# Kernel tuning notes

Hardware: AMD Instinct MI355X
Metric: run time of the kernel (lower is better)

## Reference

```python
import jax, jax.numpy as jnp
import numpy as np

N = 100_000      # nodes
E = 3_200_000    # edges (avg degree 32)
D_IN = 64        # input node feature dim == lin3 out_dim (max over x_dict)
D_EDGE = 16      # edge feature dim
H = 16           # hidden_dim (also skip1 out = 16)


def setup_inputs() -> dict:
    key = jax.random.key(0)
    ks = jax.random.split(key, 12)
    x = jax.random.normal(ks[0], (N, D_IN), dtype=jnp.float32)
    edge_index = jax.random.randint(ks[1], (2, E), 0, N, dtype=jnp.int32)
    edge_attr = jax.random.normal(ks[2], (E, D_EDGE), dtype=jnp.float32)
    s = 0.05
    # conv1: message MLP over concat(x_src, edge_attr): (D_IN+D_EDGE) -> H
    W_msg1 = jax.random.normal(ks[3], (D_IN + D_EDGE, H), dtype=jnp.float32) * s
    b_msg1 = jnp.zeros((H,), dtype=jnp.float32)
    W_skip1 = jax.random.normal(ks[4], (D_IN, H), dtype=jnp.float32) * s
    b_skip1 = jnp.zeros((H,), dtype=jnp.float32)
    # conv2: concat(h_src, edge_attr): (H+D_EDGE) -> H
    W_msg2 = jax.random.normal(ks[5], (H + D_EDGE, H), dtype=jnp.float32) * s
    b_msg2 = jnp.zeros((H,), dtype=jnp.float32)
    W_skip2 = jax.random.normal(ks[6], (H, H), dtype=jnp.float32) * s
    b_skip2 = jnp.zeros((H,), dtype=jnp.float32)
    W_lin3 = jax.random.normal(ks[7], (H, D_IN), dtype=jnp.float32) * s
    b_lin3 = jnp.zeros((D_IN,), dtype=jnp.float32)
    return {
        "x": x, "edge_index": edge_index, "edge_attr": edge_attr,
        "W_msg1": W_msg1, "b_msg1": b_msg1, "W_skip1": W_skip1, "b_skip1": b_skip1,
        "W_msg2": W_msg2, "b_msg2": b_msg2, "W_skip2": W_skip2, "b_skip2": b_skip2,
        "W_lin3": W_lin3, "b_lin3": b_lin3,
    }


def _edge_conv(h, src, dst, edge_attr, W, b, num_nodes):
    # gather -> per-edge linear -> scatter-add at destination
    m = jnp.concatenate([h[src], edge_attr], axis=-1) @ W + b  # [E, H]
    return jax.ops.segment_sum(m, dst, num_segments=num_nodes)  # [N, H]


def reference(x, edge_index, edge_attr,
              W_msg1, b_msg1, W_skip1, b_skip1,
              W_msg2, b_msg2, W_skip2, b_skip2,
              W_lin3, b_lin3):
    src, dst = edge_index[0], edge_index[1]
    n = x.shape[0]
    h = _edge_conv(x, src, dst, edge_attr, W_msg1, b_msg1, n) + (x @ W_skip1 + b_skip1)
    h = jax.nn.relu(h)
    # dropout is identity in eval mode
    h = _edge_conv(h, src, dst, edge_attr, W_msg2, b_msg2, n) + (h @ W_skip2 + b_skip2)
    return h @ W_lin3 + b_lin3  # [N, D_IN]
```

## Files before the change

### kernel.cpp

```cpp
#include <hip/hip_runtime.h>

#define D_INF 64
#define DEF 16
#define HF 16

__device__ __forceinline__ void atomAddF(float* p, float v) {
#if defined(__HIP_DEVICE_COMPILE__)
    unsafeAtomicAdd(p, v);
#else
    atomicAdd(p, v);
#endif
}

__global__ __launch_bounds__(256) void k_prep(const float* __restrict__ x,
                                              const float* __restrict__ Wm1,
                                              const float* __restrict__ Ws1,
                                              const float* __restrict__ bs1,
                                              int N, float* __restrict__ xt1, float* __restrict__ s1) {
    int t = blockIdx.x * blockDim.x + threadIdx.x;
    int n = t >> 4, f = t & 15;
    if (n >= N) return;
    const float4* xr4 = (const float4*)(x + (size_t)n * D_INF);
    float am = 0.f, as = bs1[f];
#pragma unroll
    for (int k4 = 0; k4 < 16; k4++) {
        float4 v = xr4[k4];
        int k = 4 * k4;
        am += v.x * Wm1[(k + 0) * HF + f]; as += v.x * Ws1[(k + 0) * HF + f];
        am += v.y * Wm1[(k + 1) * HF + f]; as += v.y * Ws1[(k + 1) * HF + f];
        am += v.z * Wm1[(k + 2) * HF + f]; as += v.z * Ws1[(k + 2) * HF + f];
        am += v.w * Wm1[(k + 3) * HF + f]; as += v.w * Ws1[(k + 3) * HF + f];
    }
    size_t idx = (size_t)n * HF + f;
    xt1[idx] = am;
    s1[idx]  = as;
}

__global__ __launch_bounds__(256) void k_edge1(const int* __restrict__ src, const int* __restrict__ dst,
                                               const float* __restrict__ xt1, const float* __restrict__ eattr,
                                               const float* __restrict__ b1,
                                               int E, float* __restrict__ aggm, float* __restrict__ agge) {
    long long t = (long long)blockIdx.x * blockDim.x + threadIdx.x;
    int e = (int)(t >> 4), f = (int)(t & 15);
    if (e >= E) return;
    int s = src[e], d = dst[e];
    float xv = xt1[(size_t)s * HF + f] + b1[f];
    float ev = __builtin_nontemporal_load(eattr + (size_t)e * DEF + f);
    atomAddF(aggm + (size_t)d * HF + f, xv);
    atomAddF(agge + (size_t)d * HF + f, ev);
}

__global__ __launch_bounds__(256) void k_node1(const float* __restrict__ aggm, const float* __restrict__ agge,
                                               const float* __restrict__ s1,
                                               const float* __restrict__ Wm1, const float* __restrict__ Wm2,
                                               const float* __restrict__ Ws2, const float* __restrict__ bs2,
                                               int N, float* __restrict__ xt2, float* __restrict__ h2base) {
    int t = blockIdx.x * blockDim.x + threadIdx.x;
    int n = t >> 4, f = t & 15;
    if (n >= N) return;
    size_t idx = (size_t)n * HF + f;
    float ae  = agge[idx];
    float acc = aggm[idx] + s1[idx];
#pragma unroll
    for (int k = 0; k < HF; k++) {
        acc += __shfl(ae, k, 16) * Wm1[(D_INF + k) * HF + f];
    }
    float h1 = fmaxf(acc, 0.f);
    float xv = 0.f, hb = bs2[f];
#pragma unroll
    for (int k = 0; k < HF; k++) {
        float hk = __shfl(h1, k, 16);
        float ak = __shfl(ae, k, 16);
        xv += hk * Wm2[k * HF + f];
        hb += hk * Ws2[k * HF + f];
        hb += ak * Wm2[(HF + k) * HF + f];
    }
    xt2[idx]    = xv;
    h2base[idx] = hb;
}

__global__ __launch_bounds__(256) void k_edge2(const int* __restrict__ src, const int* __restrict__ dst,
                                               const float* __restrict__ xt2, const float* __restrict__ b2,
                                               int E, float* __restrict__ agg2) {
    long long t = (long long)blockIdx.x * blockDim.x + threadIdx.x;
    int e = (int)(t >> 4), f = (int)(t & 15);
    if (e >= E) return;
    int s = src[e], d = dst[e];
    float xv = xt2[(size_t)s * HF + f] + b2[f];
    atomAddF(agg2 + (size_t)d * HF + f, xv);
}

__global__ __launch_bounds__(256) void k_node3(const float* __restrict__ agg2, const float* __restrict__ h2base,
                                               const float* __restrict__ W3, const float* __restrict__ b3,
                                               int N, float* __restrict__ out) {
    int lane = threadIdx.x & 63;
    int node = (int)((blockIdx.x * blockDim.x + threadIdx.x) >> 6);
    if (node >= N) return;
    float h2 = 0.f;
    if (lane < HF) {
        size_t idx = (size_t)node * HF + lane;
        h2 = agg2[idx] + h2base[idx];
    }
    float o = b3[lane];
#pragma unroll
    for (int k = 0; k < HF; k++) {
        o += __shfl(h2, k, 64) * W3[k * D_INF + lane];
    }
    out[(size_t)node * D_INF + lane] = o;
}


static inline size_t align256(size_t x) { return (x + 255) & ~(size_t)255; }

extern "C" void kernel_launch(void* const* d_in, const int* in_sizes, int n_in,
                              void* d_out, int out_size, void* d_ws, size_t ws_size,
                              hipStream_t stream) {
    const float* x    = (const float*)d_in[0];
    const int*   ei   = (const int*)d_in[1];
    const float* eatt = (const float*)d_in[2];
    const float* Wm1  = (const float*)d_in[3];
    const float* b1   = (const float*)d_in[4];
    const float* Ws1  = (const float*)d_in[5];
    const float* bs1  = (const float*)d_in[6];
    const float* Wm2  = (const float*)d_in[7];
    const float* b2   = (const float*)d_in[8];
    const float* Ws2  = (const float*)d_in[9];
    const float* bs2  = (const float*)d_in[10];
    const float* W3   = (const float*)d_in[11];
    const float* b3   = (const float*)d_in[12];
    float* out = (float*)d_out;

    int N = in_sizes[0] / D_INF;
    int E = in_sizes[1] / 2;
    const int* src = ei;
    const int* dst = ei + E;

    char* ws = (char*)d_ws;
    size_t off = 0;
    auto alloc = [&](size_t bytes) -> void* { void* p = ws + off; off = align256(off + bytes); return p; };

    size_t szA = (size_t)N * HF * sizeof(float);
    float* aggm   = (float*)alloc(3 * szA);
    float* agge   = aggm + (size_t)N * HF;
    float* agg2   = agge + (size_t)N * HF;
    float* xt1    = (float*)alloc(szA);
    float* s1     = (float*)alloc(szA);
    float* xt2    = (float*)alloc(szA);
    float* h2base = (float*)alloc(szA);
    (void)ws_size; (void)n_in; (void)out_size;

    hipMemsetAsync(aggm, 0, 3 * szA, stream);

    dim3 blk(256);
    int gN16 = (N * HF + 255) / 256;
    long long tE = (long long)E * HF;
    int gE16 = (int)((tE + 255) / 256);

    k_prep <<<dim3(gN16), blk, 0, stream>>>(x, Wm1, Ws1, bs1, N, xt1, s1);
    k_edge1<<<dim3(gE16), blk, 0, stream>>>(src, dst, xt1, eatt, b1, E, aggm, agge);
    k_node1<<<dim3(gN16), blk, 0, stream>>>(aggm, agge, s1, Wm1, Wm2, Ws2, bs2, N, xt2, h2base);
    k_edge2<<<dim3(gE16), blk, 0, stream>>>(src, dst, xt2, b2, E, agg2);
    k_node3<<<dim3((N + 3) / 4), blk, 0, stream>>>(agg2, h2base, W3, b3, N, out);
}
```

Measured before the change: 825.4 us.

## Build CSR by destination and replace atomic scatter-adds with per-node gather aggregation

Each call now builds a CSR grouping of edges by destination: a degree histogram, a three-kernel scan and an atomic-cursor scatter of (src, edge id) pairs. Both edge convolutions become node-centric gathers in which one wavefront sums its node's incoming messages in registers and applies the node MLPs in the same kernel. This removes the float atomics and the aggregation buffers and fuses the edge and node kernels. The cost is per-call preprocessing with int atomics plus random, uncoalesced edge_attr reads via edge ids, and the summation order is no longer deterministic.

```diff
diff --git a/kernel.cpp b/kernel.cpp
--- a/kernel.cpp
+++ b/kernel.cpp
@@ -4,12 +4,70 @@
 #define DEF 16
 #define HF 16
 
-__device__ __forceinline__ void atomAddF(float* p, float v) {
-#if defined(__HIP_DEVICE_COMPILE__)
-    unsafeAtomicAdd(p, v);
-#else
-    atomicAdd(p, v);
-#endif
+
+__global__ __launch_bounds__(256) void k_hist(const int* __restrict__ dst, int E, int* __restrict__ deg) {
+    int i = blockIdx.x * blockDim.x + threadIdx.x;
+    if (i < E) atomicAdd(&deg[dst[i]], 1);
+}
+
+#define SCAN_B 256
+__global__ __launch_bounds__(SCAN_B) void k_scan_partial(const int* __restrict__ deg, int N, int* __restrict__ partial) {
+    __shared__ int s[SCAN_B];
+    int i = blockIdx.x * SCAN_B + threadIdx.x;
+    s[threadIdx.x] = (i < N) ? deg[i] : 0;
+    __syncthreads();
+    for (int off = SCAN_B / 2; off > 0; off >>= 1) {
+        if (threadIdx.x < off) s[threadIdx.x] += s[threadIdx.x + off];
+        __syncthreads();
+    }
+    if (threadIdx.x == 0) partial[blockIdx.x] = s[0];
+}
+
+__global__ __launch_bounds__(1024) void k_scan_top(int* __restrict__ partial, int P) {
+    __shared__ int s[1024];
+    int t = threadIdx.x;
+    int orig = (t < P) ? partial[t] : 0;
+    s[t] = orig;
+    __syncthreads();
+    for (int o = 1; o < 1024; o <<= 1) {
+        int v = (t >= o) ? s[t - o] : 0;
+        __syncthreads();
+        s[t] += v;
+        __syncthreads();
+    }
+    if (t < P) partial[t] = s[t] - orig;
+}
+
+__global__ __launch_bounds__(SCAN_B) void k_scan_final(const int* __restrict__ deg, const int* __restrict__ partial,
+                                                       int N, int* __restrict__ row_ptr, int* __restrict__ cursor) {
+    __shared__ int s[SCAN_B];
+    int t = threadIdx.x;
+    int i = blockIdx.x * SCAN_B + t;
+    int d = (i < N) ? deg[i] : 0;
+    s[t] = d;
+    __syncthreads();
+    for (int o = 1; o < SCAN_B; o <<= 1) {
+        int v = (t >= o) ? s[t - o] : 0;
+        __syncthreads();
+        s[t] += v;
+        __syncthreads();
+    }
+    int excl = s[t] - d + partial[blockIdx.x];
+    if (i < N) {
+        row_ptr[i] = excl;
+        cursor[i] = excl;
+        if (i == N - 1) row_ptr[N] = excl + d;
+    }
+}
+
+__global__ __launch_bounds__(256) void k_scatter(const int* __restrict__ src, const int* __restrict__ dst, int E,
+                                                 int* __restrict__ cursor, int2* __restrict__ csr_se) {
+    int e = blockIdx.x * blockDim.x + threadIdx.x;
+    if (e < E) {
+        int d = dst[e];
+        int pos = atomicAdd(&cursor[d], 1);
+        csr_se[pos] = make_int2(src[e], e);
+    }
 }
 
 __global__ __launch_bounds__(256) void k_prep(const float* __restrict__ x,
@@ -36,31 +94,47 @@
     s1[idx]  = as;
 }
 
-__global__ __launch_bounds__(256) void k_edge1(const int* __restrict__ src, const int* __restrict__ dst,
-                                               const float* __restrict__ xt1, const float* __restrict__ eattr,
-                                               const float* __restrict__ b1,
-                                               int E, float* __restrict__ aggm, float* __restrict__ agge) {
-    long long t = (long long)blockIdx.x * blockDim.x + threadIdx.x;
-    int e = (int)(t >> 4), f = (int)(t & 15);
-    if (e >= E) return;
-    int s = src[e], d = dst[e];
-    float xv = xt1[(size_t)s * HF + f] + b1[f];
-    float ev = __builtin_nontemporal_load(eattr + (size_t)e * DEF + f);
-    atomAddF(aggm + (size_t)d * HF + f, xv);
-    atomAddF(agge + (size_t)d * HF + f, ev);
-}
-
-__global__ __launch_bounds__(256) void k_node1(const float* __restrict__ aggm, const float* __restrict__ agge,
-                                               const float* __restrict__ s1,
-                                               const float* __restrict__ Wm1, const float* __restrict__ Wm2,
-                                               const float* __restrict__ Ws2, const float* __restrict__ bs2,
-                                               int N, float* __restrict__ xt2, float* __restrict__ h2base) {
-    int t = blockIdx.x * blockDim.x + threadIdx.x;
-    int n = t >> 4, f = t & 15;
-    if (n >= N) return;
-    size_t idx = (size_t)n * HF + f;
-    float ae  = agge[idx];
-    float acc = aggm[idx] + s1[idx];
+__global__ __launch_bounds__(256) void k_conv1f(const float* __restrict__ xt1, const float* __restrict__ eattr,
+                                                const int2* __restrict__ csr_se, const int* __restrict__ row_ptr,
+                                                const float* __restrict__ s1,
+                                                const float* __restrict__ Wm1, const float* __restrict__ b1,
+                                                const float* __restrict__ Wm2,
+                                                const float* __restrict__ Ws2, const float* __restrict__ bs2,
+                                                int N, float* __restrict__ xt2, float* __restrict__ h2base) {
+    int lane = threadIdx.x & 63;
+    int node = (int)((blockIdx.x * blockDim.x + threadIdx.x) >> 6);
+    if (node >= N) return;
+    int sub = lane >> 4, f = lane & 15;
+    int r0 = row_ptr[node], r1 = row_ptr[node + 1];
+    float degf = (float)(r1 - r0);
+    float am = 0.f, ae = 0.f;
+    int j = r0 + sub;
+    for (; j + 12 < r1; j += 16) {
+        int2 se0 = csr_se[j];
+        int2 se1 = csr_se[j + 4];
+        int2 se2 = csr_se[j + 8];
+        int2 se3 = csr_se[j + 12];
+        float m0 = xt1[(size_t)se0.x * HF + f];
+        float m1 = xt1[(size_t)se1.x * HF + f];
+        float m2 = xt1[(size_t)se2.x * HF + f];
+        float m3 = xt1[(size_t)se3.x * HF + f];
+        float e0 = __builtin_nontemporal_load(eattr + (size_t)se0.y * DEF + f);
+        float e1 = __builtin_nontemporal_load(eattr + (size_t)se1.y * DEF + f);
+        float e2 = __builtin_nontemporal_load(eattr + (size_t)se2.y * DEF + f);
+        float e3 = __builtin_nontemporal_load(eattr + (size_t)se3.y * DEF + f);
+        am += (m0 + m1) + (m2 + m3);
+        ae += (e0 + e1) + (e2 + e3);
+    }
+    for (; j < r1; j += 4) {
+        int2 se = csr_se[j];
+        am += xt1[(size_t)se.x * HF + f];
+        ae += __builtin_nontemporal_load(eattr + (size_t)se.y * DEF + f);
+    }
+    am += __shfl_xor(am, 16); am += __shfl_xor(am, 32);
+    ae += __shfl_xor(ae, 16); ae += __shfl_xor(ae, 32);
+
+    size_t idx = (size_t)node * HF + f;
+    float acc = am + degf * b1[f] + s1[idx];
 #pragma unroll
     for (int k = 0; k < HF; k++) {
         acc += __shfl(ae, k, 16) * Wm1[(D_INF + k) * HF + f];
@@ -75,36 +149,41 @@
         hb += hk * Ws2[k * HF + f];
         hb += ak * Wm2[(HF + k) * HF + f];
     }
-    xt2[idx]    = xv;
-    h2base[idx] = hb;
-}
-
-__global__ __launch_bounds__(256) void k_edge2(const int* __restrict__ src, const int* __restrict__ dst,
-                                               const float* __restrict__ xt2, const float* __restrict__ b2,
-                                               int E, float* __restrict__ agg2) {
-    long long t = (long long)blockIdx.x * blockDim.x + threadIdx.x;
-    int e = (int)(t >> 4), f = (int)(t & 15);
-    if (e >= E) return;
-    int s = src[e], d = dst[e];
-    float xv = xt2[(size_t)s * HF + f] + b2[f];
-    atomAddF(agg2 + (size_t)d * HF + f, xv);
-}
-
-__global__ __launch_bounds__(256) void k_node3(const float* __restrict__ agg2, const float* __restrict__ h2base,
-                                               const float* __restrict__ W3, const float* __restrict__ b3,
-                                               int N, float* __restrict__ out) {
+    if (lane < 16) {
+        xt2[idx]    = xv;
+        h2base[idx] = hb;
+    }
+}
+
+__global__ __launch_bounds__(256) void k_conv2f(const float* __restrict__ xt2,
+                                                const int2* __restrict__ csr_se, const int* __restrict__ row_ptr,
+                                                const float* __restrict__ h2base, const float* __restrict__ b2,
+                                                const float* __restrict__ W3, const float* __restrict__ b3,
+                                                int N, float* __restrict__ out) {
     int lane = threadIdx.x & 63;
     int node = (int)((blockIdx.x * blockDim.x + threadIdx.x) >> 6);
     if (node >= N) return;
-    float h2 = 0.f;
-    if (lane < HF) {
-        size_t idx = (size_t)node * HF + lane;
-        h2 = agg2[idx] + h2base[idx];
-    }
+    int sub = lane >> 4, f = lane & 15;
+    int r0 = row_ptr[node], r1 = row_ptr[node + 1];
+    float acc = 0.f;
+    int j = r0 + sub;
+    for (; j + 12 < r1; j += 16) {
+        int s0 = csr_se[j].x;
+        int s1i = csr_se[j + 4].x;
+        int s2 = csr_se[j + 8].x;
+        int s3 = csr_se[j + 12].x;
+        acc += xt2[(size_t)s0 * HF + f] + xt2[(size_t)s1i * HF + f];
+        acc += xt2[(size_t)s2 * HF + f] + xt2[(size_t)s3 * HF + f];
+    }
+    for (; j < r1; j += 4) acc += xt2[(size_t)csr_se[j].x * HF + f];
+    acc += __shfl_xor(acc, 16);
+    acc += __shfl_xor(acc, 32);
+
+    float h2 = acc + (float)(r1 - r0) * b2[f] + h2base[(size_t)node * HF + f];
     float o = b3[lane];
 #pragma unroll
     for (int k = 0; k < HF; k++) {
-        o += __shfl(h2, k, 64) * W3[k * D_INF + lane];
+        o += __shfl(h2, k, 16) * W3[k * D_INF + lane];
     }
     out[(size_t)node * D_INF + lane] = o;
 }
@@ -139,26 +218,34 @@
     size_t off = 0;
     auto alloc = [&](size_t bytes) -> void* { void* p = ws + off; off = align256(off + bytes); return p; };
 
+    int*   deg     = (int*)alloc((size_t)N * 4);
+    int*   row_ptr = (int*)alloc((size_t)(N + 1) * 4);
+    int*   cursor  = (int*)alloc((size_t)N * 4);
+    int*   partial = (int*)alloc(1024 * 4);
+    int2*  csr_se  = (int2*)alloc((size_t)E * 8);
     size_t szA = (size_t)N * HF * sizeof(float);
-    float* aggm   = (float*)alloc(3 * szA);
-    float* agge   = aggm + (size_t)N * HF;
-    float* agg2   = agge + (size_t)N * HF;
-    float* xt1    = (float*)alloc(szA);
-    float* s1     = (float*)alloc(szA);
-    float* xt2    = (float*)alloc(szA);
-    float* h2base = (float*)alloc(szA);
+    float* xt1     = (float*)alloc(szA);
+    float* s1      = (float*)alloc(szA);
+    float* xt2     = (float*)alloc(szA);
+    float* h2base  = (float*)alloc(szA);
     (void)ws_size; (void)n_in; (void)out_size;
 
-    hipMemsetAsync(aggm, 0, 3 * szA, stream);
+    int P = (N + SCAN_B - 1) / SCAN_B;
+
+    hipMemsetAsync(deg, 0, (size_t)N * 4, stream);
 
     dim3 blk(256);
     int gN16 = (N * HF + 255) / 256;
-    long long tE = (long long)E * HF;
-    int gE16 = (int)((tE + 255) / 256);
-
-    k_prep <<<dim3(gN16), blk, 0, stream>>>(x, Wm1, Ws1, bs1, N, xt1, s1);
-    k_edge1<<<dim3(gE16), blk, 0, stream>>>(src, dst, xt1, eatt, b1, E, aggm, agge);
-    k_node1<<<dim3(gN16), blk, 0, stream>>>(aggm, agge, s1, Wm1, Wm2, Ws2, bs2, N, xt2, h2base);
-    k_edge2<<<dim3(gE16), blk, 0, stream>>>(src, dst, xt2, b2, E, agg2);
-    k_node3<<<dim3((N + 3) / 4), blk, 0, stream>>>(agg2, h2base, W3, b3, N, out);
-}
+
+    k_hist        <<<dim3((E + 255) / 256), blk, 0, stream>>>(dst, E, deg);
+    k_scan_partial<<<dim3(P), dim3(SCAN_B), 0, stream>>>(deg, N, partial);
+    k_scan_top    <<<dim3(1), dim3(1024), 0, stream>>>(partial, P);
+    k_scan_final  <<<dim3(P), dim3(SCAN_B), 0, stream>>>(deg, partial, N, row_ptr, cursor);
+    k_scatter     <<<dim3((E + 255) / 256), blk, 0, stream>>>(src, dst, E, cursor, csr_se);
+
+    k_prep  <<<dim3(gN16), blk, 0, stream>>>(x, Wm1, Ws1, bs1, N, xt1, s1);
+    k_conv1f<<<dim3((N + 3) / 4), blk, 0, stream>>>(xt1, eatt, csr_se, row_ptr, s1,
+                                                    Wm1, b1, Wm2, Ws2, bs2, N, xt2, h2base);
+    k_conv2f<<<dim3((N + 3) / 4), blk, 0, stream>>>(xt2, csr_se, row_ptr, h2base, b2,
+                                                    W3, b3, N, out);
+}
```

Result: slower. 930.8 us (+12.8%).
